# Kernel tuning notes

Measured on AMD Instinct MI355X. Metric: run time of the kernel, lower is better.

## Reference

```python
import jax, jax.numpy as jnp
import numpy as np

B, S, E = 2, 2048, 4096
H, KVH, D = 32, 8, 128          # query heads, kv heads, head_dim
GROUPS = H // KVH               # 4
WINDOW = 4096                   # sliding window (>= S -> fully causal)
ROPE_THETA = 10000.0


def _rope_sin_cos(position_ids):
    # inv_freq over even dims, freqs duplicated (Mixtral/GPT-NeoX style)
    inv_freq = 1.0 / (ROPE_THETA ** (jnp.arange(0, D, 2, dtype=jnp.float32) / D))  # [D/2]
    freqs = position_ids.astype(jnp.float32)[..., None] * inv_freq  # [B,S,D/2]
    emb = jnp.concatenate((freqs, freqs), axis=-1)                  # [B,S,D]
    # add head axis for broadcasting against [B,S,H,D]
    return jnp.sin(emb)[:, :, None, :], jnp.cos(emb)[:, :, None, :]


def _rotate_half(x):
    return jnp.concatenate((-x[..., D // 2:], x[..., :D // 2]), axis=-1)


def setup_inputs() -> dict:
    key = jax.random.key(0)
    ks = jax.random.split(key, 5)
    w_scale = 1.0 / np.sqrt(E)
    hidden_states = jax.random.normal(ks[0], (B, S, E), jnp.float32)
    Wq = jax.random.normal(ks[1], (E, H * D), jnp.float32) * w_scale
    Wk = jax.random.normal(ks[2], (E, KVH * D), jnp.float32) * w_scale
    Wv = jax.random.normal(ks[3], (E, KVH * D), jnp.float32) * w_scale
    Wo = jax.random.normal(ks[4], (H * D, E), jnp.float32) * w_scale
    # sliding-window causal mask: tril then zero entries more than WINDOW back
    causal = jnp.tril(jnp.ones((S, S), dtype=bool))
    causal = jnp.triu(causal, k=-WINDOW)[None, None]  # [1,1,S,S]
    attention_mask = jnp.ones((B, S), jnp.int32)
    position_ids = jnp.broadcast_to(jnp.arange(S, dtype=jnp.int32), (B, S))
    return dict(hidden_states=hidden_states, Wq=Wq, Wk=Wk, Wv=Wv, Wo=Wo,
                causal_mask=causal, attention_mask=attention_mask,
                position_ids=position_ids)


def reference(hidden_states, Wq, Wk, Wv, Wo, causal_mask, attention_mask, position_ids):
    # projections + head split
    q = (hidden_states @ Wq).reshape(B, S, H, D)
    k = (hidden_states @ Wk).reshape(B, S, KVH, D)
    v = (hidden_states @ Wv).reshape(B, S, KVH, D)

    # inline RoPE on q and k
    sin, cos = _rope_sin_cos(position_ids)
    q = q * cos + _rotate_half(q) * sin
    k = k * cos + _rotate_half(k) * sin

    # GQA: repeat kv heads to match query heads
    k = jnp.repeat(k, GROUPS, axis=2)  # [B,S,H,D]
    v = jnp.repeat(v, GROUPS, axis=2)

    # combined mask -> additive bias
    mask = causal_mask[:, :, :S, :S] & (attention_mask[:, None, None, :] > 0)  # [B|1,1,S,S]
    bias = jnp.where(mask, 0.0, jnp.finfo(jnp.float32).min)

    scores = jnp.einsum('bqhd,bkhd->bhqk', q, k) / jnp.sqrt(jnp.float32(D)) + bias
    probs = jax.nn.softmax(scores, axis=-1)
    attn = jnp.einsum('bhqk,bkhd->bqhd', probs, v).reshape(B, S, H * D)
    return attn @ Wo
```

## Files before the change

kernel.cpp:

```cpp
#include <hip/hip_runtime.h>
#include <hip/hip_bf16.h>
#include <cstdint>
#include <cstddef>

#define B_ 2
#define S_ 2048
#define E_ 4096
#define H_ 32
#define KVH_ 8
#define D_ 128
#define M_ (B_*S_)
#define HD_ (H_*D_)
#define KVD_ (KVH_*D_)
#define NQKV_ 6144

typedef unsigned short u16;
typedef __attribute__((ext_vector_type(8))) short bf16x8;
typedef __attribute__((ext_vector_type(4))) float f32x4;

__device__ __forceinline__ float bf2f(u16 u) {
  union { float f; uint32_t i; } v; v.i = ((uint32_t)u) << 16; return v.f;
}
__device__ __forceinline__ u16 f2bf(float f) {
  union { float f; uint32_t i; } v; v.f = f;
  uint32_t r = v.i + 0x7FFF + ((v.i >> 16) & 1);
  return (u16)(r >> 16);
}

__device__ __forceinline__ void gload_lds16(const void* g, void* l) {
  __builtin_amdgcn_global_load_lds(
      (const __attribute__((address_space(1))) void*)g,
      (__attribute__((address_space(3))) void*)l, 16, 0, 0);
}

#define FENCE() asm volatile("" ::: "memory")
#define BARRIER() do { FENCE(); __builtin_amdgcn_s_barrier(); FENCE(); } while (0)
#define VMCNT6() asm volatile("s_waitcnt vmcnt(6)" ::: "memory")

__global__ __launch_bounds__(256) void k_f2bf(const float* __restrict__ in,
                                              u16* __restrict__ out, int n) {
  int i = (blockIdx.x * 256 + threadIdx.x) * 4;
  if (i + 3 < n) {
    float4 v = *(const float4*)(in + i);
    *(ushort4*)(out + i) = make_ushort4(f2bf(v.x), f2bf(v.y), f2bf(v.z), f2bf(v.w));
  }
}

__global__ __launch_bounds__(256) void k_transpose_f2bf(const float* __restrict__ in,
                                                        u16* __restrict__ out, int R, int C) {
  __shared__ float tile[64][65];
  const int c0 = blockIdx.x * 64, r0 = blockIdx.y * 64;
  const int tid = threadIdx.x;
  const int lx = tid & 63, ty = tid >> 6;
#pragma unroll
  for (int i = 0; i < 16; ++i)
    tile[ty + 4 * i][lx] = in[(size_t)(r0 + ty + 4 * i) * C + c0 + lx];
  __syncthreads();
  const int oy = tid & 31, xb = tid >> 5;
#pragma unroll
  for (int i = 0; i < 8; ++i) {
    int X = xb + 8 * i;
    *(ushort2*)(out + (size_t)(c0 + X) * R + r0 + 2 * oy) =
        make_ushort2(f2bf(tile[2 * oy][X]), f2bf(tile[2 * oy + 1][X]));
  }
}

__global__ __launch_bounds__(256) void k_transpose_v(const u16* __restrict__ vlin,
                                                     u16* __restrict__ vt, int stride) {
  __shared__ u16 tile[64][65];
  const int bk = blockIdx.z;
  const int b = bk >> 3, kvh = bk & 7;
  const int s0 = blockIdx.x * 64, d0 = blockIdx.y * 64;
  const int tid = threadIdx.x;
  const int lx = tid & 63, ty = tid >> 6;
#pragma unroll
  for (int i = 0; i < 16; ++i)
    tile[ty + 4 * i][lx] =
        vlin[(size_t)(b * S_ + s0 + ty + 4 * i) * stride + kvh * D_ + d0 + lx];
  __syncthreads();
  const int oy = tid & 31, xb = tid >> 5;
#pragma unroll
  for (int i = 0; i < 8; ++i) {
    int X = xb + 8 * i;
    *(ushort2*)(vt + ((size_t)bk * D_ + d0 + X) * S_ + s0 + 2 * oy) =
        make_ushort2(tile[2 * oy][X], tile[2 * oy + 1][X]);
  }
}

__global__ __launch_bounds__(256) void k_table(float2* __restrict__ tab) {
  int i = blockIdx.x * 256 + threadIdx.x;
  if (i < S_ * 64) {
    int s = i >> 6, d = i & 63;
    float inv = powf(10000.0f, -(float)d / 64.0f);
    float f = (float)s * inv;
    tab[i] = make_float2(sinf(f), cosf(f));
  }
}

__global__ __launch_bounds__(256) void k_rope(const u16* __restrict__ in, u16* __restrict__ out,
                                              const float2* __restrict__ tab,
                                              const int* __restrict__ pos,
                                              int heads, int in_stride, int total) {
  int i = blockIdx.x * 256 + threadIdx.x;
  if (i >= total) return;
  int d = i & 63;
  int s = (i >> 6) & (S_ - 1);
  int bh = i >> 17;
  int h = bh % heads, b = bh / heads;
  size_t ibase = ((size_t)(b * S_ + s)) * in_stride + h * D_;
  float2 scv = tab[pos[b * S_ + s] * 64 + d];
  float x1 = bf2f(in[ibase + d]), x2 = bf2f(in[ibase + d + 64]);
  size_t obase = ((size_t)bh * S_ + s) * D_;
  out[obase + d]      = f2bf(x1 * scv.y - x2 * scv.x);
  out[obase + d + 64] = f2bf(x2 * scv.y + x1 * scv.x);
}

template<bool OUTF32>
__global__ __launch_bounds__(512, 2) void k_gemm8(const u16* __restrict__ A,
                                                  const u16* __restrict__ BT,
                                                  void* __restrict__ Cp,
                                                  int M, int N, int K) {
  __shared__ __align__(16) u16 L[8 * 8192];
  const int tid = threadIdx.x;
  const int w = tid >> 6, lane = tid & 63;
  const int lrow = lane & 15, lk = lane >> 4;
  const int nbn = N >> 8;
  const int tm = blockIdx.x / nbn, tn = blockIdx.x % nbn;
  const int m0 = tm << 8, n0 = tn << 8;
  const int wm = w >> 2, wn = w & 3;

  f32x4 acc[8][4] = {};
  bf16x8 bres[4][2];
  const int nt = K >> 6;

  const u16* RA[2] = { &L[(0 + wm) * 8192],       &L[(4 + wm) * 8192] };
  const u16* RB[2] = { &L[(2 + (wn >> 1)) * 8192], &L[(6 + (wn >> 1)) * 8192] };

  auto STAGE = [&](int buf, int mat, int half, int t) {
    const u16* src = mat ? BT : A;
    const int base0 = mat ? n0 : m0;
    u16* reg = &L[(buf * 4 + mat * 2 + half) * 8192];
#pragma unroll
    for (int c = 0; c < 2; ++c) {
      int rl = (c << 6) + (w << 3) + (lane >> 3);
      int gb = (lane & 7) ^ (rl & 7);
      gload_lds16(src + (size_t)(base0 + (half << 7) + rl) * K + (t << 6) + (gb << 3),
                  reg + ((c << 6) + (w << 3)) * 64);
    }
  };
  auto LDB = [&](int buf) {
#pragma unroll
    for (int nf = 0; nf < 4; ++nf)
#pragma unroll
      for (int ks = 0; ks < 2; ++ks) {
        int br = ((wn & 1) << 6) + (nf << 4) + lrow;
        int cb = (ks << 2) + lk;
        bres[nf][ks] = *(const bf16x8*)(RB[buf] + br * 64 + ((cb ^ (br & 7)) << 3));
      }
  };
  auto LDA2 = [&](int buf, int mp, bf16x8 (&af)[2][2]) {
#pragma unroll
    for (int d = 0; d < 2; ++d)
#pragma unroll
      for (int ks = 0; ks < 2; ++ks) {
        int ar = (((mp << 1) + d) << 4) + lrow;
        int cb = (ks << 2) + lk;
        af[d][ks] = *(const bf16x8*)(RA[buf] + ar * 64 + ((cb ^ (ar & 7)) << 3));
      }
  };
  auto MM2 = [&](int mp, bf16x8 (&af)[2][2]) {
    __builtin_amdgcn_s_setprio(1);
#pragma unroll
    for (int ks = 0; ks < 2; ++ks)
#pragma unroll
      for (int d = 0; d < 2; ++d)
#pragma unroll
        for (int nf = 0; nf < 4; ++nf)
          acc[(mp << 1) + d][nf] = __builtin_amdgcn_mfma_f32_16x16x32_bf16(
              af[d][ks], bres[nf][ks], acc[(mp << 1) + d][nf], 0, 0, 0);
    __builtin_amdgcn_s_setprio(0);
  };

  STAGE(0, 1, 0, 0); STAGE(0, 1, 1, 0);
  STAGE(0, 0, 0, 0); STAGE(0, 0, 1, 0);
  STAGE(1, 1, 0, 1); STAGE(1, 1, 1, 1);

  const int niter = nt >> 1;
  for (int i = 0; i < niter; ++i) {
    const int t1 = 2 * i + 1;
    const int t2 = (2 * i + 2 < nt) ? 2 * i + 2 : nt - 1;
    const int t3 = (2 * i + 3 < nt) ? 2 * i + 3 : nt - 1;
    bf16x8 afA[2][2], afB[2][2];

    STAGE(1, 0, 0, t1);
    VMCNT6();
    BARRIER();
    LDB(0); LDA2(0, 0, afA);
    MM2(0, afA);
    LDA2(0, 1, afB);
    BARRIER();
    STAGE(1, 0, 1, t1);
    MM2(1, afB);
    LDA2(0, 2, afA);
    BARRIER();
    STAGE(0, 1, 0, t2);
    MM2(2, afA);
    LDA2(0, 3, afB);
    BARRIER();
    STAGE(0, 1, 1, t2);
    MM2(3, afB);
    BARRIER();

    STAGE(0, 0, 0, t2);
    VMCNT6();
    BARRIER();
    LDB(1); LDA2(1, 0, afA);
    MM2(0, afA);
    LDA2(1, 1, afB);
    BARRIER();
    STAGE(0, 0, 1, t2);
    MM2(1, afB);
    LDA2(1, 2, afA);
    BARRIER();
    STAGE(1, 1, 0, t3);
    MM2(2, afA);
    LDA2(1, 3, afB);
    BARRIER();
    STAGE(1, 1, 1, t3);
    MM2(3, afB);
    BARRIER();
  }

#pragma unroll
  for (int mi = 0; mi < 8; ++mi)
#pragma unroll
    for (int nf = 0; nf < 4; ++nf) {
      int col = n0 + (wn << 6) + (nf << 4) + lrow;
#pragma unroll
      for (int j = 0; j < 4; ++j) {
        int row = m0 + (wm << 7) + (mi << 4) + (lk << 2) + j;
        if (OUTF32) ((float*)Cp)[(size_t)row * N + col] = acc[mi][nf][j];
        else        ((u16*)Cp)[(size_t)row * N + col]  = f2bf(acc[mi][nf][j]);
      }
    }
}

__global__ __launch_bounds__(512, 4) void k_attn(const u16* __restrict__ QKV,
                                                 const u16* __restrict__ Kr,
                                                 const u16* __restrict__ Vt,
                                                 const float2* __restrict__ tab,
                                                 const int* __restrict__ pos,
                                                 u16* __restrict__ ctx) {
  __shared__ __align__(16) u16 Ks[2][64 * 128];
  __shared__ __align__(16) u16 Vs[2][128 * 64];
  __shared__ __align__(16) u16 Ps[8][16 * 40];
  const int bid = blockIdx.x;
  const int qt = 15 - (bid >> 6);
  const int bh = bid & 63;
  const int b = bh >> 5, h = bh & 31;
  const int kvh = h >> 2;
  const int tid = threadIdx.x;
  const int w = tid >> 6, lane = tid & 63;
  const int lrow = lane & 15, lk = lane >> 4;
  const int q0w = qt * 128 + w * 16;

  const int s = q0w + lrow;
  const int p = pos[b * S_ + s];
  const u16* q0 = QKV + ((size_t)(b * S_ + s)) * NQKV_ + h * D_ + lk * 8;
  bf16x8 raw[4];
#pragma unroll
  for (int ks = 0; ks < 4; ++ks) raw[ks] = *(const bf16x8*)(q0 + ks * 32);
  bf16x8 qf[4];
#pragma unroll
  for (int ks = 0; ks < 2; ++ks)
#pragma unroll
    for (int e = 0; e < 8; ++e) {
      int d = ks * 32 + lk * 8 + e;
      float2 scv = tab[p * 64 + d];
      float x1 = bf2f((u16)raw[ks][e]), x2 = bf2f((u16)raw[ks + 2][e]);
      qf[ks][e]     = (short)f2bf(x1 * scv.y - x2 * scv.x);
      qf[ks + 2][e] = (short)f2bf(x2 * scv.y + x1 * scv.x);
    }

  float m[4] = {-1e30f, -1e30f, -1e30f, -1e30f};
  float l[4] = {0.f, 0.f, 0.f, 0.f};
  f32x4 o[8] = {};

  const u16* kbase = Kr + (size_t)(b * KVH_ + kvh) * S_ * D_;
  const u16* vbase = Vt + (size_t)(b * KVH_ + kvh) * D_ * S_;
  const float cl = 0.12751743435f;
  const int nt = 2 * qt + 2;

  auto STAGE = [&](int buf, int kb) {
    const int kv0 = kb << 6;
#pragma unroll
    for (int c = 0; c < 2; ++c) {
      int r = w * 8 + (lane >> 4) + c * 4;
      gload_lds16(kbase + (size_t)(kv0 + r) * D_ + (((lane & 15) ^ (r & 7)) << 3),
                  &Ks[buf][(w * 8 + c * 4) * 128]);
    }
#pragma unroll
    for (int c = 0; c < 2; ++c) {
      int r = w * 16 + (lane >> 3) + c * 8;
      gload_lds16(vbase + (size_t)r * S_ + kv0 + (((lane & 7) ^ (r & 7)) << 3),
                  &Vs[buf][(w * 16 + c * 8) * 64]);
    }
  };

  STAGE(0, 0);
  int cur = 0;
  for (int kb = 0; kb < nt; ++kb) {
    if (kb + 1 < nt) {
      STAGE(cur ^ 1, kb + 1);
      asm volatile("s_waitcnt vmcnt(4)" ::: "memory");
    } else {
      asm volatile("s_waitcnt vmcnt(0)" ::: "memory");
    }
    BARRIER();
    const int kv0 = kb << 6;
    if (kv0 <= q0w + 15) {
      const u16* Kb = &Ks[cur][0];
      const u16* Vb = &Vs[cur][0];

      f32x4 sc[4] = {};
      __builtin_amdgcn_s_setprio(1);
#pragma unroll
      for (int n0 = 0; n0 < 4; ++n0) {
#pragma unroll
        for (int ks = 0; ks < 4; ++ks) {
          int krow = (n0 << 4) + lrow;
          bf16x8 kf = *(const bf16x8*)(Kb + krow * 128 + ((((ks << 2) + lk) ^ (krow & 7)) << 3));
          sc[n0] = __builtin_amdgcn_mfma_f32_16x16x32_bf16(qf[ks], kf, sc[n0], 0, 0, 0);
        }
      }
      __builtin_amdgcn_s_setprio(0);

      const bool diag = (kv0 + 63 > q0w);
      float mnew[4] = {m[0], m[1], m[2], m[3]};
#pragma unroll
      for (int n0 = 0; n0 < 4; ++n0)
#pragma unroll
        for (int j = 0; j < 4; ++j) {
          float v = sc[n0][j] * cl;
          if (diag && (kv0 + (n0 << 4) + lrow > q0w + (lk << 2) + j)) v = -1e30f;
          sc[n0][j] = v;
          mnew[j] = fmaxf(mnew[j], v);
        }
#pragma unroll
      for (int j = 0; j < 4; ++j) {
        float v = mnew[j];
        v = fmaxf(v, __shfl_xor(v, 1));
        v = fmaxf(v, __shfl_xor(v, 2));
        v = fmaxf(v, __shfl_xor(v, 4));
        v = fmaxf(v, __shfl_xor(v, 8));
        mnew[j] = v;
      }

      bool need = false;
#pragma unroll
      for (int j = 0; j < 4; ++j) need |= (mnew[j] - m[j] > 11.5f);
      if (__any(need)) {
        float alpha[4];
#pragma unroll
        for (int j = 0; j < 4; ++j) {
          alpha[j] = exp2f(m[j] - mnew[j]);
          m[j] = mnew[j];
          l[j] *= alpha[j];
        }
#pragma unroll
        for (int db = 0; db < 8; ++db)
#pragma unroll
          for (int j = 0; j < 4; ++j)
            o[db][j] *= alpha[j];
      }

      float rs[4] = {0.f, 0.f, 0.f, 0.f};
#pragma unroll
      for (int n0 = 0; n0 < 4; ++n0)
#pragma unroll
        for (int j = 0; j < 4; ++j) {
          float pv = exp2f(sc[n0][j] - m[j]);
          sc[n0][j] = pv;
          rs[j] += pv;
        }
#pragma unroll
      for (int j = 0; j < 4; ++j) {
        float v = rs[j];
        v += __shfl_xor(v, 1); v += __shfl_xor(v, 2);
        v += __shfl_xor(v, 4); v += __shfl_xor(v, 8);
        l[j] += v;
      }

      u16* pw = &Ps[w][0];
#pragma unroll
      for (int half = 0; half < 2; ++half) {
        asm volatile("s_waitcnt lgkmcnt(0)" ::: "memory");
#pragma unroll
        for (int n0 = 0; n0 < 2; ++n0)
#pragma unroll
          for (int j = 0; j < 4; ++j)
            pw[((lk << 2) + j) * 40 + (n0 << 4) + lrow] =
                f2bf(sc[(half << 1) + n0][j]);
        bf16x8 pf = *(const bf16x8*)(pw + lrow * 40 + (lk << 3));
        __builtin_amdgcn_s_setprio(1);
#pragma unroll
        for (int db = 0; db < 8; ++db) {
          int dr = (db << 4) + lrow;
          bf16x8 vf = *(const bf16x8*)(Vb + dr * 64 + ((((half << 2) + lk) ^ (dr & 7)) << 3));
          o[db] = __builtin_amdgcn_mfma_f32_16x16x32_bf16(pf, vf, o[db], 0, 0, 0);
        }
        __builtin_amdgcn_s_setprio(0);
      }
    }
    BARRIER();
    cur ^= 1;
  }

#pragma unroll
  for (int j = 0; j < 4; ++j) l[j] = 1.0f / l[j];
#pragma unroll
  for (int db = 0; db < 8; ++db)
#pragma unroll
    for (int j = 0; j < 4; ++j) {
      int q = q0w + (lk << 2) + j;
      ctx[((size_t)(b * S_ + q)) * HD_ + h * D_ + (db << 4) + lrow] = f2bf(o[db][j] * l[j]);
    }
}

extern "C" void kernel_launch(void* const* d_in, const int* in_sizes, int n_in,
                              void* d_out, int out_size, void* d_ws, size_t ws_size,
                              hipStream_t stream) {
  const float* hidden = (const float*)d_in[0];
  const float* Wq = (const float*)d_in[1];
  const float* Wk = (const float*)d_in[2];
  const float* Wv = (const float*)d_in[3];
  const float* Wo = (const float*)d_in[4];
  const int* pos_ids = (const int*)d_in[7];

  char* ws = (char*)d_ws;
  u16* hs      = (u16*)(ws);
  u16* ctx     = hs;
  u16* wqkvt   = (u16*)(ws + 33554432ull);
  u16* wot     = wqkvt;
  u16* qkvlin  = (u16*)(ws + 83886080ull);
  u16* kr      = (u16*)(ws + 134217728ull);
  u16* vt      = (u16*)(ws + 142606336ull);
  float2* tab  = (float2*)(ws + 150994944ull);

  k_f2bf<<<dim3((M_*E_)/1024), dim3(256), 0, stream>>>(hidden, hs, M_*E_);
  k_transpose_f2bf<<<dim3(HD_/64, E_/64), dim3(256), 0, stream>>>(Wq, wqkvt, E_, HD_);
  k_transpose_f2bf<<<dim3(KVD_/64, E_/64), dim3(256), 0, stream>>>(Wk, wqkvt + (size_t)HD_*E_, E_, KVD_);
  k_transpose_f2bf<<<dim3(KVD_/64, E_/64), dim3(256), 0, stream>>>(Wv, wqkvt + (size_t)(HD_+KVD_)*E_, E_, KVD_);
  k_gemm8<false><<<dim3((M_/256)*(NQKV_/256)), dim3(512), 0, stream>>>(hs, wqkvt, (void*)qkvlin, M_, NQKV_, E_);
  k_transpose_f2bf<<<dim3(E_/64, HD_/64), dim3(256), 0, stream>>>(Wo, wot, HD_, E_);
  k_table<<<dim3((S_*64)/256), dim3(256), 0, stream>>>(tab);
  k_rope<<<dim3((B_*KVH_*S_*64)/256), dim3(256), 0, stream>>>(qkvlin + HD_, kr, tab, pos_ids, KVH_, NQKV_, B_*KVH_*S_*64);
  k_transpose_v<<<dim3(S_/64, D_/64, B_*KVH_), dim3(256), 0, stream>>>(qkvlin + HD_ + KVD_, vt, NQKV_);
  k_attn<<<dim3(B_*H_*(S_/128)), dim3(512), 0, stream>>>(qkvlin, kr, vt, tab, pos_ids, ctx);
  k_gemm8<true><<<dim3((M_/256)*(E_/256)), dim3(512), 0, stream>>>(ctx, wot, d_out, M_, E_, HD_);
}
```

Measured before the change: 587.2 us.

## Compute softmax row sums via extra MFMA ones-column and prescale Q

The attention kernel drops the per-tile row-sum reduction (adds plus four cross-lane shuffles per row) and the separate l accumulator. Instead it appends a 16-row block of V in LDS whose first row is all ones, so a ninth MFMA per half-tile accumulates the softmax denominator in o[8]. The scale constant is also folded into Q during RoPE, removing a multiply per score. The cost is one extra MFMA per half-tile, more LDS for the padded V buffers and more accumulator registers. Because the denominator now sums bf16-rounded probabilities, its numerics change slightly.

```diff
diff --git a/kernel.cpp b/kernel.cpp
--- a/kernel.cpp
+++ b/kernel.cpp
@@ -252,7 +252,7 @@
                                                  const int* __restrict__ pos,
                                                  u16* __restrict__ ctx) {
   __shared__ __align__(16) u16 Ks[2][64 * 128];
-  __shared__ __align__(16) u16 Vs[2][128 * 64];
+  __shared__ __align__(16) u16 Vs[2][144 * 64];
   __shared__ __align__(16) u16 Ps[8][16 * 40];
   const int bid = blockIdx.x;
   const int qt = 15 - (bid >> 6);
@@ -264,6 +264,7 @@
   const int lrow = lane & 15, lk = lane >> 4;
   const int q0w = qt * 128 + w * 16;
 
+  const float cl = 0.12751743435f;
   const int s = q0w + lrow;
   const int p = pos[b * S_ + s];
   const u16* q0 = QKV + ((size_t)(b * S_ + s)) * NQKV_ + h * D_ + lk * 8;
@@ -278,17 +279,15 @@
       int d = ks * 32 + lk * 8 + e;
       float2 scv = tab[p * 64 + d];
       float x1 = bf2f((u16)raw[ks][e]), x2 = bf2f((u16)raw[ks + 2][e]);
-      qf[ks][e]     = (short)f2bf(x1 * scv.y - x2 * scv.x);
-      qf[ks + 2][e] = (short)f2bf(x2 * scv.y + x1 * scv.x);
+      qf[ks][e]     = (short)f2bf(cl * (x1 * scv.y - x2 * scv.x));
+      qf[ks + 2][e] = (short)f2bf(cl * (x2 * scv.y + x1 * scv.x));
     }
 
   float m[4] = {-1e30f, -1e30f, -1e30f, -1e30f};
-  float l[4] = {0.f, 0.f, 0.f, 0.f};
-  f32x4 o[8] = {};
+  f32x4 o[9] = {};
 
   const u16* kbase = Kr + (size_t)(b * KVH_ + kvh) * S_ * D_;
   const u16* vbase = Vt + (size_t)(b * KVH_ + kvh) * D_ * S_;
-  const float cl = 0.12751743435f;
   const int nt = 2 * qt + 2;
 
   auto STAGE = [&](int buf, int kb) {
@@ -306,6 +305,13 @@
                   &Vs[buf][(w * 16 + c * 8) * 64]);
     }
   };
+
+  for (int i = tid; i < 16 * 64; i += 512) {
+    u16 v = (i < 64) ? (u16)0x3F80 : (u16)0;
+    Vs[0][128 * 64 + i] = v;
+    Vs[1][128 * 64 + i] = v;
+  }
+  asm volatile("s_waitcnt lgkmcnt(0)" ::: "memory");
 
   STAGE(0, 0);
   int cur = 0;
@@ -341,7 +347,7 @@
       for (int n0 = 0; n0 < 4; ++n0)
 #pragma unroll
         for (int j = 0; j < 4; ++j) {
-          float v = sc[n0][j] * cl;
+          float v = sc[n0][j];
           if (diag && (kv0 + (n0 << 4) + lrow > q0w + (lk << 2) + j)) v = -1e30f;
           sc[n0][j] = v;
           mnew[j] = fmaxf(mnew[j], v);
@@ -365,31 +371,19 @@
         for (int j = 0; j < 4; ++j) {
           alpha[j] = exp2f(m[j] - mnew[j]);
           m[j] = mnew[j];
-          l[j] *= alpha[j];
         }
 #pragma unroll
-        for (int db = 0; db < 8; ++db)
+        for (int db = 0; db < 9; ++db)
 #pragma unroll
           for (int j = 0; j < 4; ++j)
             o[db][j] *= alpha[j];
       }
 
-      float rs[4] = {0.f, 0.f, 0.f, 0.f};
 #pragma unroll
       for (int n0 = 0; n0 < 4; ++n0)
 #pragma unroll
-        for (int j = 0; j < 4; ++j) {
-          float pv = exp2f(sc[n0][j] - m[j]);
-          sc[n0][j] = pv;
-          rs[j] += pv;
-        }
-#pragma unroll
-      for (int j = 0; j < 4; ++j) {
-        float v = rs[j];
-        v += __shfl_xor(v, 1); v += __shfl_xor(v, 2);
-        v += __shfl_xor(v, 4); v += __shfl_xor(v, 8);
-        l[j] += v;
-      }
+        for (int j = 0; j < 4; ++j)
+          sc[n0][j] = exp2f(sc[n0][j] - m[j]);
 
       u16* pw = &Ps[w][0];
 #pragma unroll
@@ -404,7 +398,7 @@
         bf16x8 pf = *(const bf16x8*)(pw + lrow * 40 + (lk << 3));
         __builtin_amdgcn_s_setprio(1);
 #pragma unroll
-        for (int db = 0; db < 8; ++db) {
+        for (int db = 0; db < 9; ++db) {
           int dr = (db << 4) + lrow;
           bf16x8 vf = *(const bf16x8*)(Vb + dr * 64 + ((((half << 2) + lk) ^ (dr & 7)) << 3));
           o[db] = __builtin_amdgcn_mfma_f32_16x16x32_bf16(pf, vf, o[db], 0, 0, 0);
@@ -416,14 +410,15 @@
     cur ^= 1;
   }
 
-#pragma unroll
-  for (int j = 0; j < 4; ++j) l[j] = 1.0f / l[j];
+  float linv[4];
+#pragma unroll
+  for (int j = 0; j < 4; ++j) linv[j] = 1.0f / __shfl(o[8][j], lane & 48);
 #pragma unroll
   for (int db = 0; db < 8; ++db)
 #pragma unroll
     for (int j = 0; j < 4; ++j) {
       int q = q0w + (lk << 2) + j;
-      ctx[((size_t)(b * S_ + q)) * HD_ + h * D_ + (db << 4) + lrow] = f2bf(o[db][j] * l[j]);
+      ctx[((size_t)(b * S_ + q)) * HD_ + h * D_ + (db << 4) + lrow] = f2bf(o[db][j] * linv[j]);
     }
 }
 
```

New measurement: 574.5 us, median of 2. 2.2% less time.
